# Optimization experiments

Hardware: AMD Instinct MI355X
Metric: run time of the kernel (lower is better)

## Reference

```python
import jax, jax.numpy as jnp
import numpy as np

N, E, D, NUM_REL, NUM_LAYERS = 20000, 100000, 768, 7, 5  # 6 edge types + self-loop relation


def setup_inputs() -> dict:
    key = jax.random.key(0)
    ks = jax.random.split(key, 8)
    x = jax.random.normal(ks[0], (N, D), dtype=jnp.float32)
    edge_index = jax.random.randint(ks[1], (2, E), 0, N, dtype=jnp.int64)
    # original edge_type values are in [-1, 5]; module adds 1 -> [0, 6]
    edge_type = jax.random.randint(ks[2], (E,), -1, 6, dtype=jnp.int64)
    scale = 1.0 / np.sqrt(D)
    weights = jax.random.normal(ks[3], (NUM_LAYERS, NUM_REL, D, D), dtype=jnp.float32) * scale
    roots = jax.random.normal(ks[4], (NUM_LAYERS, D, D), dtype=jnp.float32) * scale
    biases = jax.random.normal(ks[5], (NUM_LAYERS, D), dtype=jnp.float32) * 0.01
    return {"x": x, "edge_index": edge_index, "edge_type": edge_type,
            "weights": weights, "roots": roots, "biases": biases}


def _rgcn_conv(h, src, dst, safe_et, W, root, b):
    # PyG RGCNConv (aggr='mean', root_weight=True, bias=True):
    #   out = x @ root + b + sum_r mean_{edges of rel r into v}(x[src]) @ W_r
    n = h.shape[0]
    hs = h[src]  # [E, D] gather once, reused across relations
    out = h @ root + b
    for r in range(NUM_REL):
        m = (safe_et == r).astype(h.dtype)  # [E]
        msg_sum = jax.ops.segment_sum(hs * m[:, None], dst, num_segments=n)  # [N, D]
        cnt = jax.ops.segment_sum(m, dst, num_segments=n)  # [N]
        mean = msg_sum / jnp.maximum(cnt, 1.0)[:, None]  # zero where no rel-r edges
        out = out + mean @ W[r]
    return out


def reference(x, edge_index, edge_type, weights, roots, biases):
    src, dst = edge_index[0], edge_index[1]
    safe_et = edge_type + 1  # [-1..5] -> [0..6]
    h = x
    for l in range(NUM_LAYERS):
        h = _rgcn_conv(h, src, dst, safe_et, weights[l], roots[l], biases[l])
        h = jax.nn.relu(h)  # dropout=0 -> identity
    return h
```

## Files before the change

kernel.cpp:

```cpp
#include <hip/hip_runtime.h>

typedef unsigned short u16;
typedef unsigned int   u32;
typedef __attribute__((ext_vector_type(8))) short short8;
typedef __attribute__((ext_vector_type(4))) float f32x4;

#define DD      768
#define KK      6144
#define NREL    7
#define NLAYERS 5

__device__ __forceinline__ float b2f(u16 v) {
  return __uint_as_float(((u32)v) << 16);
}
__device__ __forceinline__ u16 f2bf(float f) {
  u32 x = __float_as_uint(f);
  x += 0x7fffu + ((x >> 16) & 1u);
  return (u16)(x >> 16);
}
__device__ __forceinline__ void gload16(const void* g, void* l) {
  __builtin_amdgcn_global_load_lds(
      (const __attribute__((address_space(1))) void*)g,
      (__attribute__((address_space(3))) void*)l, 16, 0, 0);
}


__global__ void cast_x_kernel(const float* __restrict__ x, u16* __restrict__ H, size_t n) {
  for (size_t i = ((size_t)blockIdx.x * 256 + threadIdx.x) * 4; i < n; i += (size_t)gridDim.x * 256 * 4) {
    float4 v = *(const float4*)&x[i];
    u32 lo = (u32)f2bf(v.x) | ((u32)f2bf(v.y) << 16);
    u32 hi = (u32)f2bf(v.z) | ((u32)f2bf(v.w) << 16);
    uint2 o; o.x = lo; o.y = hi;
    *(uint2*)&H[i] = o;
  }
}

__global__ void count_kernel(const int* __restrict__ eidx, const int* __restrict__ etype,
                             int* cnt_dst, int* cnt_rel, int E, int Nn) {
  int e = blockIdx.x * 256 + threadIdx.x;
  if (e >= E) return;
  int dst = eidx[E + e];
  int rel = etype[e] + 1;
  atomicAdd(&cnt_dst[dst], 1);
  atomicAdd(&cnt_rel[(size_t)rel * Nn + dst], 1);
}

__global__ __launch_bounds__(1024) void scan_kernel(const int* __restrict__ cnt, int* __restrict__ offs, int n) {
  __shared__ int part[1024];
  int t = threadIdx.x;
  int per = (n + 1023) / 1024;
  int base = t * per;
  int s = 0;
  for (int i = 0; i < per; ++i) { int idx = base + i; if (idx < n) s += cnt[idx]; }
  part[t] = s;
  __syncthreads();
  for (int o = 1; o < 1024; o <<= 1) {
    int v = (t >= o) ? part[t - o] : 0;
    __syncthreads();
    part[t] += v;
    __syncthreads();
  }
  int excl = (t == 0) ? 0 : part[t - 1];
  s = excl;
  for (int i = 0; i < per; ++i) { int idx = base + i; if (idx < n) { offs[idx] = s; s += cnt[idx]; } }
  if (t == 1023) offs[n] = part[1023];
}

__global__ void fillperm_kernel(const int* __restrict__ eidx, const int* __restrict__ offs,
                                int* fill, int* perm, int E) {
  int e = blockIdx.x * 256 + threadIdx.x;
  if (e >= E) return;
  int dst = eidx[E + e];
  int pos = offs[dst] + atomicAdd(&fill[dst], 1);
  perm[pos] = e;
}

__global__ void wcat_kernel(const float* __restrict__ W, const float* __restrict__ R, u16* __restrict__ Bt) {
  __shared__ float t[32 * 33];
  int b = blockIdx.x;
  int s = b / 576, rem = b % 576;
  int kt = rem / 24, nt = rem % 24;
  const float* src = (s == 0) ? R : (W + (size_t)(s - 1) * DD * DD);
  int tj = threadIdx.x & 31, ti = threadIdx.x >> 5;
#pragma unroll
  for (int i = 0; i < 4; ++i) {
    int kk = kt * 32 + ti + i * 8;
    t[(ti + i * 8) * 33 + tj] = src[(size_t)kk * DD + nt * 32 + tj];
  }
  __syncthreads();
#pragma unroll
  for (int i = 0; i < 4; ++i) {
    int nn_ = nt * 32 + ti + i * 8;
    Bt[(size_t)nn_ * KK + (size_t)s * DD + kt * 32 + tj] = f2bf(t[tj * 33 + ti + i * 8]);
  }
}

__global__ void copy_h_kernel(const u16* __restrict__ Hin, u16* __restrict__ Acat, int nn) {
  size_t total = (size_t)nn * (DD / 8);
  for (size_t i = (size_t)blockIdx.x * 256 + threadIdx.x; i < total; i += (size_t)gridDim.x * 256) {
    size_t r = i / (DD / 8), c = i % (DD / 8);
    *(uint4*)&Acat[r * KK + c * 8] = *(const uint4*)&Hin[r * DD + c * 8];
  }
}

__global__ __launch_bounds__(256) void aggregate_kernel(
    const u16* __restrict__ H, const int* __restrict__ esrc, const int* __restrict__ etype,
    const int* __restrict__ offs, const int* __restrict__ perm, const int* __restrict__ cnt_rel,
    u16* __restrict__ Acat, int node0, int Nn) {
  __shared__ float acc[NREL * DD];
  int v = node0 + blockIdx.x;
  int t = threadIdx.x;
  int j0 = t * 3;
  for (int i = t; i < NREL * DD; i += 256) acc[i] = 0.f;
  __syncthreads();
  int beg = offs[v], end = offs[v + 1];
  for (int e = beg; e < end; ++e) {
    int eid = perm[e];
    int src = esrc[eid];
    int rel = etype[eid] + 1;
    const u16* hr = H + (size_t)src * DD + j0;
    float* a = acc + rel * DD + j0;
    a[0] += b2f(hr[0]);
    a[1] += b2f(hr[1]);
    a[2] += b2f(hr[2]);
  }
  __syncthreads();
  size_t rowbase = (size_t)blockIdx.x * KK;
  for (int r = 0; r < NREL; ++r) {
    int c = cnt_rel[(size_t)r * Nn + v];
    float inv = (c > 0) ? 1.f / (float)c : 0.f;
    const float* a = acc + r * DD + j0;
    u16* o = Acat + rowbase + (size_t)(r + 1) * DD + j0;
    o[0] = f2bf(a[0] * inv);
    o[1] = f2bf(a[1] * inv);
    o[2] = f2bf(a[2] * inv);
  }
}


__global__ __launch_bounds__(512, 2) void gemm256_kernel(
    const u16* __restrict__ A, const u16* __restrict__ Bt, const float* __restrict__ bias,
    u16* __restrict__ Hout, float* __restrict__ Cout, int Mvalid, int Mtiles) {
  __shared__ u16 sm[4][16384];

  int tid = threadIdx.x;
  int lane = tid & 63;
  int wv = tid >> 6;
  int wm = wv >> 2, wn = wv & 3;

  int nwg = Mtiles * 3;
  int orig = (int)blockIdx.x;
  int q8 = nwg >> 3, r8 = nwg & 7;
  int xcd = orig & 7, rank = orig >> 3;
  int wg = (xcd < r8 ? xcd * (q8 + 1) : r8 * (q8 + 1) + (xcd - r8) * q8) + rank;
  int bm = wg / 3, bn = wg % 3;

  const char* gA[2];
  const char* gB[2];
#pragma unroll
  for (int j = 0; j < 2; ++j) {
    int qq = j * 8192 + tid * 16;
    int qp = qq ^ (((qq >> 9) & 1) << 5);
    int row = ((qp >> 10) << 4) | ((qp >> 6) & 15);
    int kb  = qp & 63;
    int ra = bm * 256 + row; if (ra > Mvalid - 1) ra = Mvalid - 1;
    int rb = bn * 256 + row;
    gA[j] = (const char*)A  + (size_t)ra * (KK * 2) + kb;
    gB[j] = (const char*)Bt + (size_t)rb * (KK * 2) + kb;
  }
  int rsel = lane & 15;
  int laneoff = ((rsel * 64) + ((lane >> 4) * 16)) ^ ((rsel & 8) << 2);

  f32x4 acc[8][4];
#pragma unroll
  for (int m = 0; m < 8; ++m)
#pragma unroll
    for (int n = 0; n < 4; ++n) acc[m][n] = (f32x4){0.f, 0.f, 0.f, 0.f};

  const int NSTEP = KK / 32;

  auto STAGEA = [&](int t2, int buf) {
    size_t ko = (size_t)t2 * 64;
    char* dst = (char*)&sm[buf][0];
#pragma unroll
    for (int j = 0; j < 2; ++j)
      gload16(gA[j] + ko, dst + j * 8192 + tid * 16);
  };
  auto STAGEB = [&](int t2, int buf) {
    size_t ko = (size_t)t2 * 64;
    char* dst = (char*)&sm[buf][8192];
#pragma unroll
    for (int j = 0; j < 2; ++j)
      gload16(gB[j] + ko, dst + j * 8192 + tid * 16);
  };

  STAGEA(0, 0); STAGEB(0, 0);
  STAGEA(1, 1); STAGEB(1, 1);
  asm volatile("s_waitcnt vmcnt(4)" ::: "memory");
  __builtin_amdgcn_s_barrier();
  __builtin_amdgcn_sched_barrier(0);

  for (int t = 0; t < NSTEP; ++t) {
    int cur = t & 3;
    int nxt = (t + 2) & 3;
    const char* sa = (const char*)&sm[cur][0];
    const char* sb = (const char*)&sm[cur][8192];

    short8 a8[8], b01[2], b23[2];
#pragma unroll
    for (int m = 0; m < 8; ++m)
      a8[m] = *(const short8*)(sa + (wm * 8 + m) * 1024 + laneoff);
#pragma unroll
    for (int n = 0; n < 2; ++n)
      b01[n] = *(const short8*)(sb + (wn * 4 + n) * 1024 + laneoff);
    if (t + 2 < NSTEP) STAGEA(t + 2, nxt);
    __builtin_amdgcn_s_barrier();
    __builtin_amdgcn_s_setprio(1);
#pragma unroll
    for (int m = 0; m < 8; ++m) {
      acc[m][0] = __builtin_amdgcn_mfma_f32_16x16x32_bf16(a8[m], b01[0], acc[m][0], 0, 0, 0);
      acc[m][1] = __builtin_amdgcn_mfma_f32_16x16x32_bf16(a8[m], b01[1], acc[m][1], 0, 0, 0);
    }
    __builtin_amdgcn_s_setprio(0);
    __builtin_amdgcn_s_barrier();

#pragma unroll
    for (int n = 0; n < 2; ++n)
      b23[n] = *(const short8*)(sb + (wn * 4 + 2 + n) * 1024 + laneoff);
    if (t + 2 < NSTEP) STAGEB(t + 2, nxt);
    __builtin_amdgcn_s_barrier();
    __builtin_amdgcn_s_setprio(1);
#pragma unroll
    for (int m = 0; m < 8; ++m) {
      acc[m][2] = __builtin_amdgcn_mfma_f32_16x16x32_bf16(a8[m], b23[0], acc[m][2], 0, 0, 0);
      acc[m][3] = __builtin_amdgcn_mfma_f32_16x16x32_bf16(a8[m], b23[1], acc[m][3], 0, 0, 0);
    }
    __builtin_amdgcn_s_setprio(0);
    if (t + 3 < NSTEP) asm volatile("s_waitcnt vmcnt(4)" ::: "memory");
    else               asm volatile("s_waitcnt vmcnt(0)" ::: "memory");
    __builtin_amdgcn_s_barrier();
    __builtin_amdgcn_sched_barrier(0);
  }

  int rif = (lane >> 4) * 4;
  int cidx = lane & 15;
#pragma unroll
  for (int m = 0; m < 8; ++m) {
    int rl = bm * 256 + wm * 128 + m * 16 + rif;
#pragma unroll
    for (int n = 0; n < 4; ++n) {
      int c = bn * 256 + wn * 64 + n * 16 + cidx;
      float bv = bias[c];
#pragma unroll
      for (int j = 0; j < 4; ++j) {
        int r = rl + j;
        if (r < Mvalid) {
          float v = acc[m][n][j] + bv;
          v = v > 0.f ? v : 0.f;
          if (Hout) Hout[(size_t)r * DD + c] = f2bf(v);
          if (Cout) Cout[(size_t)r * DD + c] = v;
        }
      }
    }
  }
}


static inline size_t alignup(size_t x, size_t a) { return (x + a - 1) & ~(a - 1); }

extern "C" void kernel_launch(void* const* d_in, const int* in_sizes, int n_in,
                              void* d_out, int out_size, void* d_ws, size_t ws_size,
                              hipStream_t stream) {
  const float* x       = (const float*)d_in[0];
  const int*   eidx    = (const int*)d_in[1];
  const int*   etype   = (const int*)d_in[2];
  const float* weights = (const float*)d_in[3];
  const float* roots   = (const float*)d_in[4];
  const float* biases  = (const float*)d_in[5];
  float* out = (float*)d_out;

  const int Nn = in_sizes[0] / DD;
  const int E  = in_sizes[2];

  char* p = (char*)d_ws;
  size_t off = 0;
  auto carve = [&](size_t bytes) -> char* {
    char* r = p + off;
    off = alignup(off + bytes, 256);
    return r;
  };
  u16* H0      = (u16*)carve((size_t)Nn * DD * 2);
  u16* Bt      = (u16*)carve((size_t)DD * KK * 2);
  int* cnt_rel = (int*)carve((size_t)NREL * Nn * 4);
  int* cnt_dst = (int*)carve((size_t)Nn * 4);
  int* offs    = (int*)carve((size_t)(Nn + 1) * 4);
  int* fill    = (int*)carve((size_t)Nn * 4);
  int* perm    = (int*)carve((size_t)E * 4);

  size_t rem = (ws_size > off) ? (ws_size - off) : 0;
  int McCap = (int)(rem / ((size_t)KK * 2));
  int Mpad = ((Nn + 255) / 256) * 256;
  int Mc = (McCap < Mpad) ? (McCap & ~255) : Mpad;
  if (Mc < 256) return;
  u16* Acat = (u16*)(p + off);
  int nchunks = (Nn + Mc - 1) / Mc;
  u16* H1 = (u16*)d_out;

  (void)hipMemsetAsync(cnt_rel, 0, (size_t)NREL * Nn * 4, stream);
  (void)hipMemsetAsync(cnt_dst, 0, (size_t)Nn * 4, stream);
  (void)hipMemsetAsync(fill, 0, (size_t)Nn * 4, stream);

  int eg = (E + 255) / 256;
  count_kernel<<<eg, 256, 0, stream>>>(eidx, etype, cnt_dst, cnt_rel, E, Nn);
  scan_kernel<<<1, 1024, 0, stream>>>(cnt_dst, offs, Nn);
  fillperm_kernel<<<eg, 256, 0, stream>>>(eidx, offs, fill, perm, E);
  cast_x_kernel<<<2048, 256, 0, stream>>>(x, H0, (size_t)Nn * DD);

  const u16* Hin = H0;
  u16* Hnext = H1;
  for (int l = 0; l < NLAYERS; ++l) {
    wcat_kernel<<<8 * 576, 256, 0, stream>>>(weights + (size_t)l * NREL * DD * DD,
                                             roots + (size_t)l * DD * DD, Bt);
    for (int c = 0; c < nchunks; ++c) {
      int node0 = c * Mc;
      int nn = (Nn - node0 < Mc) ? (Nn - node0) : Mc;
      int copy16 = nn * (DD / 8);
      int cb = (copy16 + 255) / 256;
      if (cb > 2048) cb = 2048;
      copy_h_kernel<<<cb, 256, 0, stream>>>(Hin + (size_t)node0 * DD, Acat, nn);
      aggregate_kernel<<<nn, 256, 0, stream>>>(Hin, eidx, etype, offs, perm, cnt_rel,
                                               Acat, node0, Nn);
      int mt = (nn + 255) / 256;
      u16* ho = (l < NLAYERS - 1) ? (Hnext + (size_t)node0 * DD) : nullptr;
      float* co = (l == NLAYERS - 1) ? (out + (size_t)node0 * DD) : nullptr;
      gemm256_kernel<<<mt * 3, 512, 0, stream>>>(Acat, Bt, biases + (size_t)l * DD, ho, co, nn, mt);
    }
    const u16* t_ = Hin;
    Hin = Hnext;
    Hnext = (u16*)t_;
  }
}
```

Measured before the change: 1.548 ms.

## Register-accumulate aggregation and double-buffer GEMM fragments with deeper prefetch

Result: faster. 1.482 ms (-4.3%).

```diff
diff --git a/kernel.cpp b/kernel.cpp
--- a/kernel.cpp
+++ b/kernel.cpp
@@ -103,37 +103,46 @@
   }
 }
 
-__global__ __launch_bounds__(256) void aggregate_kernel(
+__global__ __launch_bounds__(192) void aggregate_kernel(
     const u16* __restrict__ H, const int* __restrict__ esrc, const int* __restrict__ etype,
     const int* __restrict__ offs, const int* __restrict__ perm, const int* __restrict__ cnt_rel,
     u16* __restrict__ Acat, int node0, int Nn) {
-  __shared__ float acc[NREL * DD];
   int v = node0 + blockIdx.x;
   int t = threadIdx.x;
-  int j0 = t * 3;
-  for (int i = t; i < NREL * DD; i += 256) acc[i] = 0.f;
-  __syncthreads();
+  int j0 = t * 4;
+  float a0[4] = {0,0,0,0}, a1[4] = {0,0,0,0}, a2[4] = {0,0,0,0}, a3[4] = {0,0,0,0};
+  float a4[4] = {0,0,0,0}, a5[4] = {0,0,0,0}, a6[4] = {0,0,0,0};
   int beg = offs[v], end = offs[v + 1];
   for (int e = beg; e < end; ++e) {
     int eid = perm[e];
     int src = esrc[eid];
     int rel = etype[eid] + 1;
-    const u16* hr = H + (size_t)src * DD + j0;
-    float* a = acc + rel * DD + j0;
-    a[0] += b2f(hr[0]);
-    a[1] += b2f(hr[1]);
-    a[2] += b2f(hr[2]);
-  }
-  __syncthreads();
+    uint2 w = *(const uint2*)&H[(size_t)src * DD + j0];
+    float f0 = b2f((u16)(w.x & 0xffff));
+    float f1 = b2f((u16)(w.x >> 16));
+    float f2 = b2f((u16)(w.y & 0xffff));
+    float f3 = b2f((u16)(w.y >> 16));
+    switch (rel) {
+      case 0: a0[0]+=f0; a0[1]+=f1; a0[2]+=f2; a0[3]+=f3; break;
+      case 1: a1[0]+=f0; a1[1]+=f1; a1[2]+=f2; a1[3]+=f3; break;
+      case 2: a2[0]+=f0; a2[1]+=f1; a2[2]+=f2; a2[3]+=f3; break;
+      case 3: a3[0]+=f0; a3[1]+=f1; a3[2]+=f2; a3[3]+=f3; break;
+      case 4: a4[0]+=f0; a4[1]+=f1; a4[2]+=f2; a4[3]+=f3; break;
+      case 5: a5[0]+=f0; a5[1]+=f1; a5[2]+=f2; a5[3]+=f3; break;
+      default: a6[0]+=f0; a6[1]+=f1; a6[2]+=f2; a6[3]+=f3; break;
+    }
+  }
   size_t rowbase = (size_t)blockIdx.x * KK;
+  const float* regs[NREL] = {a0, a1, a2, a3, a4, a5, a6};
+#pragma unroll
   for (int r = 0; r < NREL; ++r) {
     int c = cnt_rel[(size_t)r * Nn + v];
     float inv = (c > 0) ? 1.f / (float)c : 0.f;
-    const float* a = acc + r * DD + j0;
-    u16* o = Acat + rowbase + (size_t)(r + 1) * DD + j0;
-    o[0] = f2bf(a[0] * inv);
-    o[1] = f2bf(a[1] * inv);
-    o[2] = f2bf(a[2] * inv);
+    const float* a = regs[r];
+    u32 lo = (u32)f2bf(a[0] * inv) | ((u32)f2bf(a[1] * inv) << 16);
+    u32 hi = (u32)f2bf(a[2] * inv) | ((u32)f2bf(a[3] * inv) << 16);
+    uint2 o; o.x = lo; o.y = hi;
+    *(uint2*)&Acat[rowbase + (size_t)(r + 1) * DD + j0] = o;
   }
 }
 
@@ -163,10 +172,8 @@
     int qp = qq ^ (((qq >> 9) & 1) << 5);
     int row = ((qp >> 10) << 4) | ((qp >> 6) & 15);
     int kb  = qp & 63;
-    int ra = bm * 256 + row; if (ra > Mvalid - 1) ra = Mvalid - 1;
-    int rb = bn * 256 + row;
-    gA[j] = (const char*)A  + (size_t)ra * (KK * 2) + kb;
-    gB[j] = (const char*)Bt + (size_t)rb * (KK * 2) + kb;
+    gA[j] = (const char*)A  + (size_t)(bm * 256 + row) * (KK * 2) + kb;
+    gB[j] = (const char*)Bt + (size_t)(bn * 256 + row) * (KK * 2) + kb;
   }
   int rsel = lane & 15;
   int laneoff = ((rsel * 64) + ((lane >> 4) * 16)) ^ ((rsel & 8) << 2);
@@ -179,68 +186,69 @@
 
   const int NSTEP = KK / 32;
 
-  auto STAGEA = [&](int t2, int buf) {
-    size_t ko = (size_t)t2 * 64;
-    char* dst = (char*)&sm[buf][0];
-#pragma unroll
-    for (int j = 0; j < 2; ++j)
-      gload16(gA[j] + ko, dst + j * 8192 + tid * 16);
-  };
-  auto STAGEB = [&](int t2, int buf) {
-    size_t ko = (size_t)t2 * 64;
-    char* dst = (char*)&sm[buf][8192];
-#pragma unroll
-    for (int j = 0; j < 2; ++j)
-      gload16(gB[j] + ko, dst + j * 8192 + tid * 16);
-  };
-
-  STAGEA(0, 0); STAGEB(0, 0);
-  STAGEA(1, 1); STAGEB(1, 1);
+#define STAGE(t2)                                                        \
+  do {                                                                   \
+    int s_ = (t2) & 3;                                                   \
+    size_t ko_ = (size_t)(t2) * 64;                                      \
+    char* d_ = (char*)&sm[s_][0];                                        \
+    gload16(gA[0] + ko_, d_ + tid * 16);                                 \
+    gload16(gA[1] + ko_, d_ + 8192 + tid * 16);                          \
+    gload16(gB[0] + ko_, d_ + 16384 + tid * 16);                         \
+    gload16(gB[1] + ko_, d_ + 16384 + 8192 + tid * 16);                  \
+  } while (0)
+
+#define READF(t2, ar, br)                                                \
+  do {                                                                   \
+    const char* base_ = (const char*)&sm[(t2) & 3][0];                   \
+    _Pragma("unroll")                                                    \
+    for (int m = 0; m < 8; ++m)                                          \
+      ar[m] = *(const short8*)(base_ + (wm * 8 + m) * 1024 + laneoff);   \
+    _Pragma("unroll")                                                    \
+    for (int n = 0; n < 4; ++n)                                          \
+      br[n] = *(const short8*)(base_ + 16384 + (wn * 4 + n) * 1024 + laneoff); \
+  } while (0)
+
+#define MFMA32(ar, br)                                                   \
+  do {                                                                   \
+    _Pragma("unroll")                                                    \
+    for (int m = 0; m < 8; ++m)                                          \
+      _Pragma("unroll")                                                  \
+      for (int n = 0; n < 4; ++n)                                        \
+        acc[m][n] = __builtin_amdgcn_mfma_f32_16x16x32_bf16(ar[m], br[n], acc[m][n], 0, 0, 0); \
+  } while (0)
+
+  short8 aE[8], bE[4], aO[8], bO[4];
+
+  STAGE(0); STAGE(1); STAGE(2);
   asm volatile("s_waitcnt vmcnt(4)" ::: "memory");
   __builtin_amdgcn_s_barrier();
   __builtin_amdgcn_sched_barrier(0);
-
-  for (int t = 0; t < NSTEP; ++t) {
-    int cur = t & 3;
-    int nxt = (t + 2) & 3;
-    const char* sa = (const char*)&sm[cur][0];
-    const char* sb = (const char*)&sm[cur][8192];
-
-    short8 a8[8], b01[2], b23[2];
-#pragma unroll
-    for (int m = 0; m < 8; ++m)
-      a8[m] = *(const short8*)(sa + (wm * 8 + m) * 1024 + laneoff);
-#pragma unroll
-    for (int n = 0; n < 2; ++n)
-      b01[n] = *(const short8*)(sb + (wn * 4 + n) * 1024 + laneoff);
-    if (t + 2 < NSTEP) STAGEA(t + 2, nxt);
-    __builtin_amdgcn_s_barrier();
+  READF(0, aE, bE);
+
+  for (int t = 0; t < NSTEP; t += 2) {
+    if (t + 3 < NSTEP) STAGE(t + 3);
+    READF(t + 1, aO, bO);
+    __builtin_amdgcn_sched_barrier(0);
     __builtin_amdgcn_s_setprio(1);
-#pragma unroll
-    for (int m = 0; m < 8; ++m) {
-      acc[m][0] = __builtin_amdgcn_mfma_f32_16x16x32_bf16(a8[m], b01[0], acc[m][0], 0, 0, 0);
-      acc[m][1] = __builtin_amdgcn_mfma_f32_16x16x32_bf16(a8[m], b01[1], acc[m][1], 0, 0, 0);
-    }
+    MFMA32(aE, bE);
     __builtin_amdgcn_s_setprio(0);
-    __builtin_amdgcn_s_barrier();
-
-#pragma unroll
-    for (int n = 0; n < 2; ++n)
-      b23[n] = *(const short8*)(sb + (wn * 4 + 2 + n) * 1024 + laneoff);
-    if (t + 2 < NSTEP) STAGEB(t + 2, nxt);
-    __builtin_amdgcn_s_barrier();
-    __builtin_amdgcn_s_setprio(1);
-#pragma unroll
-    for (int m = 0; m < 8; ++m) {
-      acc[m][2] = __builtin_amdgcn_mfma_f32_16x16x32_bf16(a8[m], b23[0], acc[m][2], 0, 0, 0);
-      acc[m][3] = __builtin_amdgcn_mfma_f32_16x16x32_bf16(a8[m], b23[1], acc[m][3], 0, 0, 0);
-    }
-    __builtin_amdgcn_s_setprio(0);
-    if (t + 3 < NSTEP) asm volatile("s_waitcnt vmcnt(4)" ::: "memory");
-    else               asm volatile("s_waitcnt vmcnt(0)" ::: "memory");
+    asm volatile("s_waitcnt vmcnt(4)" ::: "memory");
     __builtin_amdgcn_s_barrier();
     __builtin_amdgcn_sched_barrier(0);
-  }
+
+    if (t + 4 < NSTEP) STAGE(t + 4);
+    if (t + 2 < NSTEP) READF(t + 2, aE, bE);
+    __builtin_amdgcn_sched_barrier(0);
+    __builtin_amdgcn_s_setprio(1);
+    MFMA32(aO, bO);
+    __builtin_amdgcn_s_setprio(0);
+    asm volatile("s_waitcnt vmcnt(4)" ::: "memory");
+    __builtin_amdgcn_s_barrier();
+    __builtin_amdgcn_sched_barrier(0);
+  }
+#undef STAGE
+#undef READF
+#undef MFMA32
 
   int rif = (lane >> 4) * 4;
   int cidx = lane & 15;
@@ -328,7 +336,7 @@
       int cb = (copy16 + 255) / 256;
       if (cb > 2048) cb = 2048;
       copy_h_kernel<<<cb, 256, 0, stream>>>(Hin + (size_t)node0 * DD, Acat, nn);
-      aggregate_kernel<<<nn, 256, 0, stream>>>(Hin, eidx, etype, offs, perm, cnt_rel,
+      aggregate_kernel<<<nn, 192, 0, stream>>>(Hin, eidx, etype, offs, perm, cnt_rel,
                                                Acat, node0, Nn);
       int mt = (nn + 255) / 256;
       u16* ho = (l < NLAYERS - 1) ? (Hnext + (size_t)node0 * DD) : nullptr;
```
